# Performance work log

Hardware: AMD Instinct MI355X
Metric: run time of the kernel (lower is better)

## Reference

```python
import jax, jax.numpy as jnp
import numpy as np

N = 25000      # nodes
E = 400000     # edges (before self loops)
G = 64         # graphs in batch
H = 16         # attention heads
ITER = 10      # stacked main GATv2 layers


def setup_inputs():
    key = jax.random.key(0)
    c = [0]
    def nk():
        c[0] += 1
        return jax.random.fold_in(key, c[0])
    def glorot(shape):
        fan = shape[-2] + shape[-1]
        return jax.random.normal(nk(), shape, jnp.float32) * np.float32(np.sqrt(2.0 / fan))
    inp = {
        "x": jax.random.normal(nk(), (N, 2), jnp.float32),
        "edge_attr": jax.random.normal(nk(), (E, 2), jnp.float32),
        "edge_index": jax.random.randint(nk(), (2, E), 0, N, jnp.int32),
        "mask": jax.random.randint(nk(), (N,), 0, 2, jnp.int32),
        "batch": jnp.sort(jax.random.randint(nk(), (N,), 0, G, jnp.int32)),
        # gcn: GATv2Conv(2, 4, heads=16, edge_dim=2), concat -> 64
        "g0_Wl": glorot((2, 64)), "g0_bl": jnp.zeros((64,), jnp.float32),
        "g0_Wr": glorot((2, 64)), "g0_br": jnp.zeros((64,), jnp.float32),
        "g0_We": glorot((2, 64)), "g0_att": glorot((H, 4)),
        "g0_bias": jnp.zeros((64,), jnp.float32),
        "bn_gamma": jnp.ones((64,), jnp.float32),
        "bn_beta": jnp.zeros((64,), jnp.float32),
        "m_Wl": glorot((ITER, 64, 64)), "m_bl": jnp.zeros((ITER, 64), jnp.float32),
        "m_Wr": glorot((ITER, 64, 64)), "m_br": jnp.zeros((ITER, 64), jnp.float32),
        "m_We": glorot((ITER, 2, 64)), "m_att": glorot((ITER, H, 4)),
        "m_bias": jnp.zeros((ITER, 64), jnp.float32),
        # final: GATv2Conv(64, 1, heads=16, concat=False)
        "f_Wl": glorot((64, 16)), "f_bl": jnp.zeros((16,), jnp.float32),
        "f_Wr": glorot((64, 16)), "f_br": jnp.zeros((16,), jnp.float32),
        "f_We": glorot((2, 16)), "f_att": glorot((H, 1)),
        "f_bias": jnp.zeros((1,), jnp.float32),
        # sbs: GATv2Conv(64, 1, heads=16, concat=False)
        "s_Wl": glorot((64, 16)), "s_bl": jnp.zeros((16,), jnp.float32),
        "s_Wr": glorot((64, 16)), "s_br": jnp.zeros((16,), jnp.float32),
        "s_We": glorot((2, 16)), "s_att": glorot((H, 1)),
        "s_bias": jnp.zeros((1,), jnp.float32),
    }
    return inp


def _gatv2(x, src, dst, eattr, Wl, bl, Wr, br, We, att, bias, concat):
    """PyG GATv2Conv: x_l[j]+x_r[i]+e -> LeakyReLU(0.2) -> att dot -> segment softmax over dst."""
    n = x.shape[0]
    h, c = att.shape
    xl = (x @ Wl + bl).reshape(n, h, c)
    xr = (x @ Wr + br).reshape(n, h, c)
    e = (eattr @ We).reshape(-1, h, c)
    m = jax.nn.leaky_relu(xl[src] + xr[dst] + e, 0.2)          # [Etot,H,C]
    logit = jnp.einsum('ehc,hc->eh', m, att)                    # [Etot,H]
    lmax = jax.ops.segment_max(logit, dst, num_segments=n)
    ex = jnp.exp(logit - lmax[dst])
    den = jax.ops.segment_sum(ex, dst, num_segments=n)
    alpha = ex / den[dst]
    out = jax.ops.segment_sum(xl[src] * alpha[..., None], dst, num_segments=n)  # [N,H,C]
    out = out.reshape(n, h * c) if concat else out.mean(axis=1)
    return out + bias


def reference(x, edge_attr, edge_index, mask, batch,
              g0_Wl, g0_bl, g0_Wr, g0_br, g0_We, g0_att, g0_bias,
              bn_gamma, bn_beta,
              m_Wl, m_bl, m_Wr, m_br, m_We, m_att, m_bias,
              f_Wl, f_bl, f_Wr, f_br, f_We, f_att, f_bias,
              s_Wl, s_bl, s_Wr, s_br, s_We, s_att, s_bias):
    n = x.shape[0]
    src, dst = edge_index[0], edge_index[1]
    # add self loops; self-loop edge attr = mean of incoming edge attrs (fill_value='mean')
    ones = jnp.ones((src.shape[0],), jnp.float32)
    cnt = jax.ops.segment_sum(ones, dst, num_segments=n)
    esum = jax.ops.segment_sum(edge_attr, dst, num_segments=n)
    loop_attr = esum / jnp.maximum(cnt, 1.0)[:, None]
    arng = jnp.arange(n, dtype=edge_index.dtype)
    src2 = jnp.concatenate([src, arng])
    dst2 = jnp.concatenate([dst, arng])
    ea2 = jnp.concatenate([edge_attr, loop_attr], axis=0)

    h0 = _gatv2(x, src2, dst2, ea2, g0_Wl, g0_bl, g0_Wr, g0_br, g0_We, g0_att, g0_bias, True)
    mu = h0.mean(axis=0)
    var = h0.var(axis=0)
    h = jax.nn.leaky_relu((h0 - mu) * jax.lax.rsqrt(var + 1e-5) * bn_gamma + bn_beta, 0.01)

    def step(hc, p):
        Wl, bl, Wr, br, We, att, bias = p
        hc = jax.nn.leaky_relu(_gatv2(hc, src2, dst2, ea2, Wl, bl, Wr, br, We, att, bias, True), 0.01)
        return hc, None
    h, _ = jax.lax.scan(step, h, (m_Wl, m_bl, m_Wr, m_br, m_We, m_att, m_bias))

    mus = _gatv2(h, src2, dst2, ea2, s_Wl, s_bl, s_Wr, s_br, s_We, s_att, s_bias, False)[:, 0]  # [N]
    fin = _gatv2(h, src2, dst2, ea2, f_Wl, f_bl, f_Wr, f_br, f_We, f_att, f_bias, False)        # [N,1]
    w = (mask == 0).astype(jnp.float32)
    sums = jax.ops.segment_sum(fin * w[:, None], batch, num_segments=G)
    cnts = jax.ops.segment_sum(w, batch, num_segments=G)
    sat = (sums / jnp.maximum(cnts, 1.0)[:, None])[:, 0]  # [G]
    return mus, sat
```

## Files before the change

### kernel.cpp

```cpp
#include <hip/hip_runtime.h>


static __device__ __forceinline__ float lrelu(float x, float s) {
    return x > 0.f ? x : s * x;
}

__global__ void k_build0(const int* __restrict__ dst, int* __restrict__ cnt,
                         int* __restrict__ rank, int E,
                         const float* __restrict__ x,
                         const float* __restrict__ Wl, const float* __restrict__ bl,
                         const float* __restrict__ Wr, const float* __restrict__ br,
                         float* __restrict__ xl, float* __restrict__ xr, int n) {
    int idx = blockIdx.x * blockDim.x + threadIdx.x;
    if (idx < E) {
        rank[idx] = atomicAdd(&cnt[dst[idx]], 1);
    } else {
        int t = idx - E;
        if (t < n * 64) {
            int i = t >> 6, c = t & 63;
            float x0 = x[2 * i], x1 = x[2 * i + 1];
            xl[t] = x0 * Wl[c] + x1 * Wl[64 + c] + bl[c];
            xr[t] = x0 * Wr[c] + x1 * Wr[64 + c] + br[c];
        }
    }
}

__global__ void k_segoff(const int* __restrict__ cnt, int* __restrict__ row_start,
                         int* __restrict__ cursor, int n) {
    int i = blockIdx.x * blockDim.x + threadIdx.x;
    int lane = threadIdx.x & 63;
    int v = (i < n) ? cnt[i] : 0;
    int s = v;
#pragma unroll
    for (int off = 1; off < 64; off <<= 1) {
        int t = __shfl_up(s, off);
        if (lane >= off) s += t;
    }
    int wavetot = __shfl(s, 63);
    int base = 0;
    if (lane == 63) base = atomicAdd(cursor, wavetot);
    base = __shfl(base, 63);
    if (i < n) row_start[i] = base + s - v;
}

__global__ void k_scatter(const int* __restrict__ src, const int* __restrict__ dst,
                          const float* __restrict__ ea, const int* __restrict__ rank,
                          const int* __restrict__ row_start,
                          int* __restrict__ csr_src, float* __restrict__ csr_ea, int E) {
    int e = blockIdx.x * blockDim.x + threadIdx.x;
    if (e >= E) return;
    int pos = row_start[dst[e]] + rank[e];
    csr_src[pos] = src[e];
    *(float2*)(csr_ea + 2 * (size_t)pos) = *(const float2*)(ea + 2 * (size_t)e);
}

__launch_bounds__(256)
__global__ void k_proj64(const float* __restrict__ h,
                         const float* __restrict__ Wl, const float* __restrict__ bl,
                         const float* __restrict__ Wr, const float* __restrict__ br,
                         const double* __restrict__ stats,
                         const float* __restrict__ bng, const float* __restrict__ bnb,
                         float* __restrict__ xl, float* __restrict__ xr, int n) {
    __shared__ float wsl[4096], wsr[4096], bna[64], bnbb[64];
    int t = threadIdx.x;
    for (int i = t; i < 4096; i += 256) { wsl[i] = Wl[i]; wsr[i] = Wr[i]; }
    if (t < 64) {
        double mu = stats[t] / n;
        double var = stats[64 + t] / n - mu * mu;
        float rs = (float)(1.0 / sqrt(var + 1e-5));
        float a = rs * bng[t];
        bna[t] = a;
        bnbb[t] = bnb[t] - (float)mu * a;
    }
    __syncthreads();
    int rg = t >> 2, cg4 = (t & 3) << 4;
    int r0 = blockIdx.x * 128 + rg * 2;
    float accl[2][16], accr[2][16];
#pragma unroll
    for (int r = 0; r < 2; ++r)
#pragma unroll
        for (int j = 0; j < 16; ++j) { accl[r][j] = 0.f; accr[r][j] = 0.f; }
    for (int k0 = 0; k0 < 64; k0 += 4) {
        float hk[2][4];
#pragma unroll
        for (int r = 0; r < 2; ++r) {
            int gr = r0 + r;
            float4 v = (gr < n) ? *(const float4*)(h + (size_t)gr * 64 + k0)
                                : make_float4(0.f, 0.f, 0.f, 0.f);
            hk[r][0] = v.x; hk[r][1] = v.y; hk[r][2] = v.z; hk[r][3] = v.w;
#pragma unroll
            for (int kk = 0; kk < 4; ++kk)
                hk[r][kk] = lrelu(hk[r][kk] * bna[k0 + kk] + bnbb[k0 + kk], 0.01f);
        }
#pragma unroll
        for (int kk = 0; kk < 4; ++kk) {
            const float* wl = wsl + (k0 + kk) * 64 + cg4;
            const float* wr = wsr + (k0 + kk) * 64 + cg4;
#pragma unroll
            for (int r = 0; r < 2; ++r)
#pragma unroll
                for (int j = 0; j < 16; ++j) {
                    accl[r][j] += hk[r][kk] * wl[j];
                    accr[r][j] += hk[r][kk] * wr[j];
                }
        }
    }
#pragma unroll
    for (int r = 0; r < 2; ++r) {
        int gr = r0 + r;
        if (gr < n) {
            float* ol = xl + (size_t)gr * 64 + cg4;
            float* orr = xr + (size_t)gr * 64 + cg4;
#pragma unroll
            for (int j = 0; j < 16; ++j) {
                ol[j] = accl[r][j] + bl[cg4 + j];
                orr[j] = accr[r][j] + br[cg4 + j];
            }
        }
    }
}

__device__ __forceinline__ float gat_node(const float* __restrict__ xl,
                                          const float* __restrict__ xr,
                                          const int* __restrict__ row_start,
                                          const int* __restrict__ cnt,
                                          const int* __restrict__ csr_src,
                                          const float* __restrict__ csr_ea,
                                          const float* __restrict__ We,
                                          const float* __restrict__ att,
                                          const float* __restrict__ bias,
                                          int d, int lane, int relu) {
    const int p0 = __builtin_amdgcn_readfirstlane(row_start[d]);
    const int deg = __builtin_amdgcn_readfirstlane(cnt[d]);
    const int p1 = p0 + deg;
    const float we0 = We[lane], we1 = We[64 + lane];
    const float av = att[lane];
    const float xrv = xr[(size_t)d * 64 + lane];

    float den0 = 0.f, acc0 = 0.f;
    float den1 = 0.f, acc1 = 0.f;
    float s0 = 0.f, s1 = 0.f;

    auto step = [&](float xv, float2 ea, bool valid, float& den, float& acc) {
        float vm = valid ? 1.f : 0.f;
        s0 = fmaf(vm, ea.x, s0);
        s1 = fmaf(vm, ea.y, s1);
        float tv = lrelu(xv + xrv + ea.x * we0 + ea.y * we1, 0.2f) * av;
        tv += __shfl_xor(tv, 1);
        tv += __shfl_xor(tv, 2);
        if (!valid) tv = -__builtin_inff();
        float w = __expf(tv);
        den += w;
        acc += w * xv;
    };

    for (int p = p0; p < p1; p += 4) {
        int q1 = min(p + 1, p1 - 1), q2 = min(p + 2, p1 - 1), q3 = min(p + 3, p1 - 1);
        int e0s = csr_src[p], e1s = csr_src[q1], e2s = csr_src[q2], e3s = csr_src[q3];
        float2 e0 = *(const float2*)(csr_ea + 2 * (size_t)p);
        float2 e1 = *(const float2*)(csr_ea + 2 * (size_t)q1);
        float2 e2 = *(const float2*)(csr_ea + 2 * (size_t)q2);
        float2 e3 = *(const float2*)(csr_ea + 2 * (size_t)q3);
        float x0 = xl[(size_t)e0s * 64 + lane];
        float x1 = xl[(size_t)e1s * 64 + lane];
        float x2 = xl[(size_t)e2s * 64 + lane];
        float x3 = xl[(size_t)e3s * 64 + lane];
        step(x0, e0, true, den0, acc0);
        step(x1, e1, p + 1 < p1, den1, acc1);
        step(x2, e2, p + 2 < p1, den0, acc0);
        step(x3, e3, p + 3 < p1, den1, acc1);
    }
    {
        float c = fmaxf((float)deg, 1.f);
        float se0 = s0 / c, se1 = s1 / c;
        float xv = xl[(size_t)d * 64 + lane];
        float tv = lrelu(xv + xrv + se0 * we0 + se1 * we1, 0.2f) * av;
        tv += __shfl_xor(tv, 1);
        tv += __shfl_xor(tv, 2);
        float w = __expf(tv);
        den0 += w;
        acc0 += w * xv;
    }
    float o = (acc0 + acc1) / (den0 + den1) + bias[lane];
    if (relu) o = lrelu(o, 0.01f);
    return o;
}

__launch_bounds__(256)
__global__ void k_gat(const float* __restrict__ xl, const float* __restrict__ xr,
                      const int* __restrict__ row_start, const int* __restrict__ cnt,
                      const int* __restrict__ csr_src, const float* __restrict__ csr_ea,
                      const float* __restrict__ We, const float* __restrict__ att,
                      const float* __restrict__ bias,
                      float* __restrict__ out, int n, int relu) {
    int wave = (blockIdx.x * blockDim.x + threadIdx.x) >> 6;
    int lane = threadIdx.x & 63;
    if (wave >= n) return;
    float o = gat_node(xl, xr, row_start, cnt, csr_src, csr_ea, We, att, bias, wave, lane, relu);
    out[(size_t)wave * 64 + lane] = o;
}

__launch_bounds__(256, 8)
__global__ void k_gat_proj2(const float* __restrict__ xl, const float* __restrict__ xr,
                            const int* __restrict__ row_start, const int* __restrict__ cnt,
                            const int* __restrict__ csr_src, const float* __restrict__ csr_ea,
                            const float* __restrict__ We, const float* __restrict__ att,
                            const float* __restrict__ bias,
                            const float* __restrict__ Wnl, const float* __restrict__ bnl,
                            const float* __restrict__ Wnr, const float* __restrict__ bnr,
                            float* __restrict__ xl_out, float* __restrict__ xr_out, int n) {
    int wave = (blockIdx.x * blockDim.x + threadIdx.x) >> 6;
    int lane = threadIdx.x & 63;
    int d0 = wave * 2, d1 = d0 + 1;
    if (d0 >= n) return;
    float o0 = gat_node(xl, xr, row_start, cnt, csr_src, csr_ea, We, att, bias, d0, lane, 1);
    float o1 = (d1 < n)
                   ? gat_node(xl, xr, row_start, cnt, csr_src, csr_ea, We, att, bias, d1, lane, 1)
                   : 0.f;
    float al0a = 0.f, al0b = 0.f, ar0a = 0.f, ar0b = 0.f;
    float al1a = 0.f, al1b = 0.f, ar1a = 0.f, ar1b = 0.f;
#pragma unroll 4
    for (int k = 0; k < 64; k += 2) {
        float h0a = __shfl(o0, k), h0b = __shfl(o0, k + 1);
        float h1a = __shfl(o1, k), h1b = __shfl(o1, k + 1);
        float wl0 = Wnl[k * 64 + lane], wl1 = Wnl[(k + 1) * 64 + lane];
        float wr0 = Wnr[k * 64 + lane], wr1 = Wnr[(k + 1) * 64 + lane];
        al0a += h0a * wl0; al0b += h0b * wl1;
        ar0a += h0a * wr0; ar0b += h0b * wr1;
        al1a += h1a * wl0; al1b += h1b * wl1;
        ar1a += h1a * wr0; ar1b += h1b * wr1;
    }
    float bL = bnl[lane], bR = bnr[lane];
    xl_out[(size_t)d0 * 64 + lane] = al0a + al0b + bL;
    xr_out[(size_t)d0 * 64 + lane] = ar0a + ar0b + bR;
    if (d1 < n) {
        xl_out[(size_t)d1 * 64 + lane] = al1a + al1b + bL;
        xr_out[(size_t)d1 * 64 + lane] = ar1a + ar1b + bR;
    }
}

__launch_bounds__(256, 8)
__global__ void k_gat_projfin2(const float* __restrict__ xl, const float* __restrict__ xr,
                               const int* __restrict__ row_start, const int* __restrict__ cnt,
                               const int* __restrict__ csr_src, const float* __restrict__ csr_ea,
                               const float* __restrict__ We, const float* __restrict__ att,
                               const float* __restrict__ bias,
                               const float* __restrict__ fWl, const float* __restrict__ fbl,
                               const float* __restrict__ fWr, const float* __restrict__ fbr,
                               const float* __restrict__ sWl, const float* __restrict__ sbl,
                               const float* __restrict__ sWr, const float* __restrict__ sbr,
                               float* __restrict__ packed, int n) {
    int wave = (blockIdx.x * blockDim.x + threadIdx.x) >> 6;
    int lane = threadIdx.x & 63;
    int d0 = wave * 2, d1 = d0 + 1;
    if (d0 >= n) return;
    float o0 = gat_node(xl, xr, row_start, cnt, csr_src, csr_ea, We, att, bias, d0, lane, 1);
    float o1 = (d1 < n)
                   ? gat_node(xl, xr, row_start, cnt, csr_src, csr_ea, We, att, bias, d1, lane, 1)
                   : 0.f;
    int q = lane >> 4, cc = lane & 15;
    const float* W = (q == 0) ? fWl : (q == 1) ? sWl : (q == 2) ? fWr : sWr;
    const float* B = (q == 0) ? fbl : (q == 1) ? sbl : (q == 2) ? fbr : sbr;
    float a0 = 0.f, a1 = 0.f, b0 = 0.f, b1 = 0.f;
#pragma unroll 4
    for (int k = 0; k < 64; k += 2) {
        float w0 = W[k * 16 + cc], w1 = W[(k + 1) * 16 + cc];
        a0 += __shfl(o0, k) * w0;
        a1 += __shfl(o0, k + 1) * w1;
        b0 += __shfl(o1, k) * w0;
        b1 += __shfl(o1, k + 1) * w1;
    }
    float bb = B[cc];
    packed[(size_t)d0 * 64 + lane] = a0 + a1 + bb;
    if (d1 < n) packed[(size_t)d1 * 64 + lane] = b0 + b1 + bb;
}

__launch_bounds__(256)
__global__ void k_gat_final(const float* __restrict__ packed,
                            const int* __restrict__ row_start, const int* __restrict__ cnt,
                            const int* __restrict__ csr_src, const float* __restrict__ csr_ea,
                            const float* __restrict__ fWe, const float* __restrict__ sWe,
                            const float* __restrict__ fatt, const float* __restrict__ satt,
                            const float* __restrict__ fbias, const float* __restrict__ sbias,
                            float* __restrict__ fin, float* __restrict__ mus, int n) {
    int hw = (blockIdx.x * blockDim.x + threadIdx.x) >> 5;
    if (hw >= n) return;
    int l = threadIdx.x & 31;
    int hh = l & 15, sel = l >> 4;
    const int d = hw;
    const int p0 = row_start[d], deg = cnt[d], p1 = p0 + deg;
    const float* We = sel ? sWe : fWe;
    float we0 = We[hh], we1 = We[16 + hh];
    float av = (sel ? satt : fatt)[hh];
    float xrv = packed[(size_t)d * 64 + 32 + sel * 16 + hh];
    int xli = sel * 16 + hh;

    float den0 = 0.f, acc0 = 0.f;
    float den1 = 0.f, acc1 = 0.f;
    float s0 = 0.f, s1 = 0.f;

    auto step = [&](float xv, float2 ea, bool valid, float& den, float& acc) {
        float vm = valid ? 1.f : 0.f;
        s0 = fmaf(vm, ea.x, s0);
        s1 = fmaf(vm, ea.y, s1);
        float t = lrelu(xv + xrv + ea.x * we0 + ea.y * we1, 0.2f) * av;
        if (!valid) t = -__builtin_inff();
        float w = __expf(t);
        den += w;
        acc += w * xv;
    };

    for (int p = p0; p < p1; p += 4) {
        int q1 = min(p + 1, p1 - 1), q2 = min(p + 2, p1 - 1), q3 = min(p + 3, p1 - 1);
        int e0s = csr_src[p], e1s = csr_src[q1], e2s = csr_src[q2], e3s = csr_src[q3];
        float2 e0 = *(const float2*)(csr_ea + 2 * (size_t)p);
        float2 e1 = *(const float2*)(csr_ea + 2 * (size_t)q1);
        float2 e2 = *(const float2*)(csr_ea + 2 * (size_t)q2);
        float2 e3 = *(const float2*)(csr_ea + 2 * (size_t)q3);
        float x0 = packed[(size_t)e0s * 64 + xli];
        float x1 = packed[(size_t)e1s * 64 + xli];
        float x2 = packed[(size_t)e2s * 64 + xli];
        float x3 = packed[(size_t)e3s * 64 + xli];
        step(x0, e0, true, den0, acc0);
        step(x1, e1, p + 1 < p1, den1, acc1);
        step(x2, e2, p + 2 < p1, den0, acc0);
        step(x3, e3, p + 3 < p1, den1, acc1);
    }
    {
        float c = fmaxf((float)deg, 1.f);
        float se0 = s0 / c, se1 = s1 / c;
        float xv = packed[(size_t)d * 64 + xli];
        float t = lrelu(xv + xrv + se0 * we0 + se1 * we1, 0.2f) * av;
        float w = __expf(t);
        den0 += w;
        acc0 += w * xv;
    }
    float val = (acc0 + acc1) / (den0 + den1);
#pragma unroll
    for (int w = 1; w < 16; w <<= 1) val += __shfl_xor(val, w);
    if ((threadIdx.x & 15) == 0) {
        float o = val * (1.f / 16.f) + (sel ? sbias[0] : fbias[0]);
        if (sel) mus[d] = o; else fin[d] = o;
    }
}


__global__ void k_bnstats(const float* __restrict__ h, double* __restrict__ stats, int n) {
    int c = threadIdx.x & 63;
    int s0 = blockIdx.x * (blockDim.x >> 6) + (threadIdx.x >> 6);
    int ns = gridDim.x * (blockDim.x >> 6);
    double s = 0.0, s2 = 0.0;
    for (int i = s0; i < n; i += ns) {
        float v = h[(size_t)i * 64 + c];
        s += v;
        s2 += (double)v * v;
    }
    atomicAdd(&stats[c], s);
    atomicAdd(&stats[64 + c], s2);
}


__global__ void k_sat_acc(const float* __restrict__ fin, const int* __restrict__ mask,
                          const int* __restrict__ batch,
                          float* __restrict__ sums, float* __restrict__ cnts, int n) {
    int i = blockIdx.x * blockDim.x + threadIdx.x;
    int lane = threadIdx.x & 63;
    int g = (i < n) ? batch[i] : -1;
    float c = (i < n && mask[i] == 0) ? 1.f : 0.f;
    float v = (c > 0.f) ? fin[i] : 0.f;
#pragma unroll
    for (int off = 1; off < 64; off <<= 1) {
        float v2 = __shfl_down(v, off);
        float c2 = __shfl_down(c, off);
        int g2 = __shfl_down(g, off);
        if (lane + off < 64 && g2 == g) { v += v2; c += c2; }
    }
    int gprev = __shfl_up(g, 1);
    bool head = (lane == 0) || (gprev != g);
    if (head && g >= 0 && c > 0.f) {
        atomicAdd(&sums[g], v);
        atomicAdd(&cnts[g], c);
    }
}

__global__ void k_sat_fin(const float* __restrict__ sums, const float* __restrict__ cnts,
                          float* __restrict__ out, int g) {
    int i = threadIdx.x;
    if (i < g) out[i] = sums[i] / fmaxf(cnts[i], 1.f);
}


extern "C" void kernel_launch(void* const* d_in, const int* in_sizes, int n_in,
                              void* d_out, int out_size, void* d_ws, size_t ws_size,
                              hipStream_t stream) {
    const float* x = (const float*)d_in[0];
    const float* eat = (const float*)d_in[1];
    const int* ei = (const int*)d_in[2];
    const int* mask = (const int*)d_in[3];
    const int* batch = (const int*)d_in[4];
    const float* g0_Wl = (const float*)d_in[5];
    const float* g0_bl = (const float*)d_in[6];
    const float* g0_Wr = (const float*)d_in[7];
    const float* g0_br = (const float*)d_in[8];
    const float* g0_We = (const float*)d_in[9];
    const float* g0_att = (const float*)d_in[10];
    const float* g0_bias = (const float*)d_in[11];
    const float* bn_g = (const float*)d_in[12];
    const float* bn_b = (const float*)d_in[13];
    const float* m_Wl = (const float*)d_in[14];
    const float* m_bl = (const float*)d_in[15];
    const float* m_Wr = (const float*)d_in[16];
    const float* m_br = (const float*)d_in[17];
    const float* m_We = (const float*)d_in[18];
    const float* m_att = (const float*)d_in[19];
    const float* m_bias = (const float*)d_in[20];
    const float* f_Wl = (const float*)d_in[21];
    const float* f_bl = (const float*)d_in[22];
    const float* f_Wr = (const float*)d_in[23];
    const float* f_br = (const float*)d_in[24];
    const float* f_We = (const float*)d_in[25];
    const float* f_att = (const float*)d_in[26];
    const float* f_bias = (const float*)d_in[27];
    const float* s_Wl = (const float*)d_in[28];
    const float* s_bl = (const float*)d_in[29];
    const float* s_Wr = (const float*)d_in[30];
    const float* s_br = (const float*)d_in[31];
    const float* s_We = (const float*)d_in[32];
    const float* s_att = (const float*)d_in[33];
    const float* s_bias = (const float*)d_in[34];

    const int N = in_sizes[3];
    const int E = in_sizes[1] / 2;
    const int G = out_size - N;
    const int ITER = in_sizes[14] / 4096;
    const int* srcp = ei;
    const int* dstp = ei + E;

    char* wsb = (char*)d_ws;
    size_t off = 0;
    auto alloc = [&](size_t b) { void* p = wsb + off; off = (off + b + 255) & ~(size_t)255; return p; };
    int* cnt = (int*)alloc((size_t)N * 4);
    int* cursor = (int*)alloc(256);
    double* stats = (double*)alloc(128 * 8);
    float* sums = (float*)alloc((size_t)G * 4);
    float* cnts = (float*)alloc((size_t)G * 4);
    size_t zero_bytes = off;
    int* rank = (int*)alloc((size_t)E * 4);
    int* row_start = (int*)alloc((size_t)N * 4);
    int* csr_src = (int*)alloc((size_t)E * 4);
    float* csr_ea = (float*)alloc((size_t)E * 8);
    float* xlA = (float*)alloc((size_t)N * 256);
    float* xrA = (float*)alloc((size_t)N * 256);
    float* xlB = (float*)alloc((size_t)N * 256);
    float* xrB = (float*)alloc((size_t)N * 256);
    float* hbuf = (float*)alloc((size_t)N * 256);
    float* fin = (float*)alloc((size_t)N * 4);
    (void)ws_size; (void)n_in;

    float* outv = (float*)d_out;

    hipMemsetAsync(d_ws, 0, zero_bytes, stream);
    const int tb = 256;
    const int ggrid = (N * 64 + 255) / 256;
    const int npair = (N + 1) / 2;
    const int ggrid2 = (npair * 64 + 255) / 256;
    k_build0<<<(E + N * 64 + tb - 1) / tb, tb, 0, stream>>>(dstp, cnt, rank, E,
                                                            x, g0_Wl, g0_bl, g0_Wr, g0_br,
                                                            xlA, xrA, N);
    k_segoff<<<(N + tb - 1) / tb, tb, 0, stream>>>(cnt, row_start, cursor, N);
    k_scatter<<<(E + tb - 1) / tb, tb, 0, stream>>>(srcp, dstp, eat, rank, row_start,
                                                    csr_src, csr_ea, E);

    k_gat<<<ggrid, tb, 0, stream>>>(xlA, xrA, row_start, cnt, csr_src, csr_ea,
                                    g0_We, g0_att, g0_bias, hbuf, N, 0);
    k_bnstats<<<128, 256, 0, stream>>>(hbuf, stats, N);
    k_proj64<<<(N + 127) / 128, 256, 0, stream>>>(hbuf, m_Wl, m_bl, m_Wr, m_br,
                                                  stats, bn_g, bn_b, xlA, xrA, N);

    float* cur_l = xlA; float* cur_r = xrA;
    float* alt_l = xlB; float* alt_r = xrB;
    for (int l = 0; l < ITER; ++l) {
        if (l < ITER - 1) {
            k_gat_proj2<<<ggrid2, tb, 0, stream>>>(cur_l, cur_r, row_start, cnt, csr_src, csr_ea,
                                                   m_We + l * 128, m_att + l * 64, m_bias + l * 64,
                                                   m_Wl + (size_t)(l + 1) * 4096, m_bl + (l + 1) * 64,
                                                   m_Wr + (size_t)(l + 1) * 4096, m_br + (l + 1) * 64,
                                                   alt_l, alt_r, N);
        } else {
            k_gat_projfin2<<<ggrid2, tb, 0, stream>>>(cur_l, cur_r, row_start, cnt, csr_src, csr_ea,
                                                      m_We + l * 128, m_att + l * 64, m_bias + l * 64,
                                                      f_Wl, f_bl, f_Wr, f_br,
                                                      s_Wl, s_bl, s_Wr, s_br,
                                                      alt_l, N);
        }
        float* t;
        t = cur_l; cur_l = alt_l; alt_l = t;
        t = cur_r; cur_r = alt_r; alt_r = t;
    }
    k_gat_final<<<(N * 32 + tb - 1) / tb, tb, 0, stream>>>(cur_l, row_start, cnt, csr_src, csr_ea,
                                                           f_We, s_We, f_att, s_att,
                                                           f_bias, s_bias, fin, outv, N);
    k_sat_acc<<<(N + tb - 1) / tb, tb, 0, stream>>>(fin, mask, batch, sums, cnts, N);
    k_sat_fin<<<1, 64, 0, stream>>>(sums, cnts, outv + N, G);
}
```

Before: 630.2 us.

## Interleave edge loops of two destination nodes per wave for more memory parallelism

Replaces the per-node aggregation with a two-node routine that walks the edge lists of both destinations in lockstep, issuing eight independent gathers per iteration instead of four. The aim is more memory-level parallelism to hide gather latency in the GAT layers. The first layer also switches to two nodes per wave, and the leaky ReLU becomes a branchless max. In exchange the loop runs to the larger of the two degrees with masked work, uses more registers, and pads the CSR arrays with a sentinel entry.

```diff
diff --git a/kernel.cpp b/kernel.cpp
--- a/kernel.cpp
+++ b/kernel.cpp
@@ -2,7 +2,7 @@
 
 
 static __device__ __forceinline__ float lrelu(float x, float s) {
-    return x > 0.f ? x : s * x;
+    return fmaxf(x, s * x);
 }
 
 __global__ void k_build0(const int* __restrict__ dst, int* __restrict__ cnt,
@@ -48,6 +48,11 @@
                           const int* __restrict__ row_start,
                           int* __restrict__ csr_src, float* __restrict__ csr_ea, int E) {
     int e = blockIdx.x * blockDim.x + threadIdx.x;
+    if (blockIdx.x == 0 && threadIdx.x == 0) {
+        csr_src[E] = 0;
+        csr_ea[2 * (size_t)E] = 0.f;
+        csr_ea[2 * (size_t)E + 1] = 0.f;
+    }
     if (e >= E) return;
     int pos = row_start[dst[e]] + rank[e];
     csr_src[pos] = src[e];
@@ -120,7 +125,7 @@
     }
 }
 
-__device__ __forceinline__ float gat_node(const float* __restrict__ xl,
+__device__ __forceinline__ void gat_node2(const float* __restrict__ xl,
                                           const float* __restrict__ xr,
                                           const int* __restrict__ row_start,
                                           const int* __restrict__ cnt,
@@ -129,19 +134,23 @@
                                           const float* __restrict__ We,
                                           const float* __restrict__ att,
                                           const float* __restrict__ bias,
-                                          int d, int lane, int relu) {
-    const int p0 = __builtin_amdgcn_readfirstlane(row_start[d]);
-    const int deg = __builtin_amdgcn_readfirstlane(cnt[d]);
-    const int p1 = p0 + deg;
+                                          int d0, int d1, int lane, int relu,
+                                          float& out0, float& out1) {
+    const int p0a = __builtin_amdgcn_readfirstlane(row_start[d0]);
+    const int dega = __builtin_amdgcn_readfirstlane(cnt[d0]);
+    const int p0b = __builtin_amdgcn_readfirstlane(row_start[d1]);
+    const int degb = __builtin_amdgcn_readfirstlane(cnt[d1]);
+    const int p1a = p0a + dega, p1b = p0b + degb;
     const float we0 = We[lane], we1 = We[64 + lane];
     const float av = att[lane];
-    const float xrv = xr[(size_t)d * 64 + lane];
-
-    float den0 = 0.f, acc0 = 0.f;
-    float den1 = 0.f, acc1 = 0.f;
-    float s0 = 0.f, s1 = 0.f;
-
-    auto step = [&](float xv, float2 ea, bool valid, float& den, float& acc) {
+    const float xrva = xr[((size_t)d0 << 6) + lane];
+    const float xrvb = xr[((size_t)d1 << 6) + lane];
+
+    float denA0 = 0.f, accA0 = 0.f, denA1 = 0.f, accA1 = 0.f, sA0 = 0.f, sA1 = 0.f;
+    float denB0 = 0.f, accB0 = 0.f, denB1 = 0.f, accB1 = 0.f, sB0 = 0.f, sB1 = 0.f;
+
+    auto step = [&](float xv, float xrv, float2 ea, bool valid,
+                    float& den, float& acc, float& s0, float& s1) {
         float vm = valid ? 1.f : 0.f;
         s0 = fmaf(vm, ea.x, s0);
         s1 = fmaf(vm, ea.y, s1);
@@ -154,50 +163,80 @@
         acc += w * xv;
     };
 
-    for (int p = p0; p < p1; p += 4) {
-        int q1 = min(p + 1, p1 - 1), q2 = min(p + 2, p1 - 1), q3 = min(p + 3, p1 - 1);
-        int e0s = csr_src[p], e1s = csr_src[q1], e2s = csr_src[q2], e3s = csr_src[q3];
-        float2 e0 = *(const float2*)(csr_ea + 2 * (size_t)p);
-        float2 e1 = *(const float2*)(csr_ea + 2 * (size_t)q1);
-        float2 e2 = *(const float2*)(csr_ea + 2 * (size_t)q2);
-        float2 e3 = *(const float2*)(csr_ea + 2 * (size_t)q3);
-        float x0 = xl[(size_t)e0s * 64 + lane];
-        float x1 = xl[(size_t)e1s * 64 + lane];
-        float x2 = xl[(size_t)e2s * 64 + lane];
-        float x3 = xl[(size_t)e3s * 64 + lane];
-        step(x0, e0, true, den0, acc0);
-        step(x1, e1, p + 1 < p1, den1, acc1);
-        step(x2, e2, p + 2 < p1, den0, acc0);
-        step(x3, e3, p + 3 < p1, den1, acc1);
+    const int iters = max(dega, degb);
+    for (int base = 0; base < iters; base += 4) {
+        const int pa = p0a + base, pb = p0b + base;
+        int ia[4], ib[4];
+        float2 ea4[4], eb4[4];
+#pragma unroll
+        for (int j = 0; j < 4; ++j) {
+            int qa = max(min(pa + j, p1a - 1), p0a);
+            int qb = max(min(pb + j, p1b - 1), p0b);
+            ia[j] = csr_src[qa];
+            ib[j] = csr_src[qb];
+            ea4[j] = *(const float2*)(csr_ea + 2 * (size_t)qa);
+            eb4[j] = *(const float2*)(csr_ea + 2 * (size_t)qb);
+        }
+        float xa[4], xb[4];
+#pragma unroll
+        for (int j = 0; j < 4; ++j) {
+            xa[j] = xl[(unsigned)((ia[j] << 6) + lane)];
+            xb[j] = xl[(unsigned)((ib[j] << 6) + lane)];
+        }
+        step(xa[0], xrva, ea4[0], base + 0 < dega, denA0, accA0, sA0, sA1);
+        step(xb[0], xrvb, eb4[0], base + 0 < degb, denB0, accB0, sB0, sB1);
+        step(xa[1], xrva, ea4[1], base + 1 < dega, denA1, accA1, sA0, sA1);
+        step(xb[1], xrvb, eb4[1], base + 1 < degb, denB1, accB1, sB0, sB1);
+        step(xa[2], xrva, ea4[2], base + 2 < dega, denA0, accA0, sA0, sA1);
+        step(xb[2], xrvb, eb4[2], base + 2 < degb, denB0, accB0, sB0, sB1);
+        step(xa[3], xrva, ea4[3], base + 3 < dega, denA1, accA1, sA0, sA1);
+        step(xb[3], xrvb, eb4[3], base + 3 < degb, denB1, accB1, sB0, sB1);
     }
     {
-        float c = fmaxf((float)deg, 1.f);
-        float se0 = s0 / c, se1 = s1 / c;
-        float xv = xl[(size_t)d * 64 + lane];
-        float tv = lrelu(xv + xrv + se0 * we0 + se1 * we1, 0.2f) * av;
+        float c = fmaxf((float)dega, 1.f);
+        float se0 = sA0 / c, se1 = sA1 / c;
+        float xv = xl[((size_t)d0 << 6) + lane];
+        float tv = lrelu(xv + xrva + se0 * we0 + se1 * we1, 0.2f) * av;
         tv += __shfl_xor(tv, 1);
         tv += __shfl_xor(tv, 2);
         float w = __expf(tv);
-        den0 += w;
-        acc0 += w * xv;
-    }
-    float o = (acc0 + acc1) / (den0 + den1) + bias[lane];
-    if (relu) o = lrelu(o, 0.01f);
-    return o;
-}
-
-__launch_bounds__(256)
-__global__ void k_gat(const float* __restrict__ xl, const float* __restrict__ xr,
-                      const int* __restrict__ row_start, const int* __restrict__ cnt,
-                      const int* __restrict__ csr_src, const float* __restrict__ csr_ea,
-                      const float* __restrict__ We, const float* __restrict__ att,
-                      const float* __restrict__ bias,
-                      float* __restrict__ out, int n, int relu) {
+        denA0 += w;
+        accA0 += w * xv;
+    }
+    {
+        float c = fmaxf((float)degb, 1.f);
+        float se0 = sB0 / c, se1 = sB1 / c;
+        float xv = xl[((size_t)d1 << 6) + lane];
+        float tv = lrelu(xv + xrvb + se0 * we0 + se1 * we1, 0.2f) * av;
+        tv += __shfl_xor(tv, 1);
+        tv += __shfl_xor(tv, 2);
+        float w = __expf(tv);
+        denB0 += w;
+        accB0 += w * xv;
+    }
+    float o0 = (accA0 + accA1) / (denA0 + denA1) + bias[lane];
+    float o1 = (accB0 + accB1) / (denB0 + denB1) + bias[lane];
+    if (relu) { o0 = lrelu(o0, 0.01f); o1 = lrelu(o1, 0.01f); }
+    out0 = o0;
+    out1 = o1;
+}
+
+__launch_bounds__(256, 8)
+__global__ void k_gat2(const float* __restrict__ xl, const float* __restrict__ xr,
+                       const int* __restrict__ row_start, const int* __restrict__ cnt,
+                       const int* __restrict__ csr_src, const float* __restrict__ csr_ea,
+                       const float* __restrict__ We, const float* __restrict__ att,
+                       const float* __restrict__ bias,
+                       float* __restrict__ out, int n, int relu) {
     int wave = (blockIdx.x * blockDim.x + threadIdx.x) >> 6;
     int lane = threadIdx.x & 63;
-    if (wave >= n) return;
-    float o = gat_node(xl, xr, row_start, cnt, csr_src, csr_ea, We, att, bias, wave, lane, relu);
-    out[(size_t)wave * 64 + lane] = o;
+    int d0 = wave * 2;
+    if (d0 >= n) return;
+    int d1 = min(d0 + 1, n - 1);
+    float o0, o1;
+    gat_node2(xl, xr, row_start, cnt, csr_src, csr_ea, We, att, bias, d0, d1, lane, relu, o0, o1);
+    out[((size_t)d0 << 6) + lane] = o0;
+    if (d0 + 1 < n) out[((size_t)d1 << 6) + lane] = o1;
 }
 
 __launch_bounds__(256, 8)
@@ -211,12 +250,11 @@
                             float* __restrict__ xl_out, float* __restrict__ xr_out, int n) {
     int wave = (blockIdx.x * blockDim.x + threadIdx.x) >> 6;
     int lane = threadIdx.x & 63;
-    int d0 = wave * 2, d1 = d0 + 1;
+    int d0 = wave * 2;
     if (d0 >= n) return;
-    float o0 = gat_node(xl, xr, row_start, cnt, csr_src, csr_ea, We, att, bias, d0, lane, 1);
-    float o1 = (d1 < n)
-                   ? gat_node(xl, xr, row_start, cnt, csr_src, csr_ea, We, att, bias, d1, lane, 1)
-                   : 0.f;
+    int d1 = min(d0 + 1, n - 1);
+    float o0, o1;
+    gat_node2(xl, xr, row_start, cnt, csr_src, csr_ea, We, att, bias, d0, d1, lane, 1, o0, o1);
     float al0a = 0.f, al0b = 0.f, ar0a = 0.f, ar0b = 0.f;
     float al1a = 0.f, al1b = 0.f, ar1a = 0.f, ar1b = 0.f;
 #pragma unroll 4
@@ -231,11 +269,11 @@
         ar1a += h1a * wr0; ar1b += h1b * wr1;
     }
     float bL = bnl[lane], bR = bnr[lane];
-    xl_out[(size_t)d0 * 64 + lane] = al0a + al0b + bL;
-    xr_out[(size_t)d0 * 64 + lane] = ar0a + ar0b + bR;
-    if (d1 < n) {
-        xl_out[(size_t)d1 * 64 + lane] = al1a + al1b + bL;
-        xr_out[(size_t)d1 * 64 + lane] = ar1a + ar1b + bR;
+    xl_out[((size_t)d0 << 6) + lane] = al0a + al0b + bL;
+    xr_out[((size_t)d0 << 6) + lane] = ar0a + ar0b + bR;
+    if (d0 + 1 < n) {
+        xl_out[((size_t)d1 << 6) + lane] = al1a + al1b + bL;
+        xr_out[((size_t)d1 << 6) + lane] = ar1a + ar1b + bR;
     }
 }
 
@@ -252,12 +290,11 @@
                                float* __restrict__ packed, int n) {
     int wave = (blockIdx.x * blockDim.x + threadIdx.x) >> 6;
     int lane = threadIdx.x & 63;
-    int d0 = wave * 2, d1 = d0 + 1;
+    int d0 = wave * 2;
     if (d0 >= n) return;
-    float o0 = gat_node(xl, xr, row_start, cnt, csr_src, csr_ea, We, att, bias, d0, lane, 1);
-    float o1 = (d1 < n)
-                   ? gat_node(xl, xr, row_start, cnt, csr_src, csr_ea, We, att, bias, d1, lane, 1)
-                   : 0.f;
+    int d1 = min(d0 + 1, n - 1);
+    float o0, o1;
+    gat_node2(xl, xr, row_start, cnt, csr_src, csr_ea, We, att, bias, d0, d1, lane, 1, o0, o1);
     int q = lane >> 4, cc = lane & 15;
     const float* W = (q == 0) ? fWl : (q == 1) ? sWl : (q == 2) ? fWr : sWr;
     const float* B = (q == 0) ? fbl : (q == 1) ? sbl : (q == 2) ? fbr : sbr;
@@ -271,8 +308,8 @@
         b1 += __shfl(o1, k + 1) * w1;
     }
     float bb = B[cc];
-    packed[(size_t)d0 * 64 + lane] = a0 + a1 + bb;
-    if (d1 < n) packed[(size_t)d1 * 64 + lane] = b0 + b1 + bb;
+    packed[((size_t)d0 << 6) + lane] = a0 + a1 + bb;
+    if (d0 + 1 < n) packed[((size_t)d1 << 6) + lane] = b0 + b1 + bb;
 }
 
 __launch_bounds__(256)
@@ -447,8 +484,8 @@
     size_t zero_bytes = off;
     int* rank = (int*)alloc((size_t)E * 4);
     int* row_start = (int*)alloc((size_t)N * 4);
-    int* csr_src = (int*)alloc((size_t)E * 4);
-    float* csr_ea = (float*)alloc((size_t)E * 8);
+    int* csr_src = (int*)alloc((size_t)(E + 4) * 4);
+    float* csr_ea = (float*)alloc((size_t)(E + 4) * 8);
     float* xlA = (float*)alloc((size_t)N * 256);
     float* xrA = (float*)alloc((size_t)N * 256);
     float* xlB = (float*)alloc((size_t)N * 256);
@@ -461,7 +498,6 @@
 
     hipMemsetAsync(d_ws, 0, zero_bytes, stream);
     const int tb = 256;
-    const int ggrid = (N * 64 + 255) / 256;
     const int npair = (N + 1) / 2;
     const int ggrid2 = (npair * 64 + 255) / 256;
     k_build0<<<(E + N * 64 + tb - 1) / tb, tb, 0, stream>>>(dstp, cnt, rank, E,
@@ -471,8 +507,8 @@
     k_scatter<<<(E + tb - 1) / tb, tb, 0, stream>>>(srcp, dstp, eat, rank, row_start,
                                                     csr_src, csr_ea, E);
 
-    k_gat<<<ggrid, tb, 0, stream>>>(xlA, xrA, row_start, cnt, csr_src, csr_ea,
-                                    g0_We, g0_att, g0_bias, hbuf, N, 0);
+    k_gat2<<<ggrid2, tb, 0, stream>>>(xlA, xrA, row_start, cnt, csr_src, csr_ea,
+                                      g0_We, g0_att, g0_bias, hbuf, N, 0);
     k_bnstats<<<128, 256, 0, stream>>>(hbuf, stats, N);
     k_proj64<<<(N + 127) / 128, 256, 0, stream>>>(hbuf, m_Wl, m_bl, m_Wr, m_br,
                                                   stats, bn_g, bn_b, xlA, xrA, N);
```

Result: slower. 663.2 us (+5.2%).

## Fuse first-layer projection into GAT0 and launch main layers with 64-thread blocks

Applied to the files above, without the earlier changes.

The first GATv2 layer now computes the 2-to-64 projections on the fly from the raw 2-dim node features inside a new k_gat0 kernel. This removes the separate xl/xr materialization in k_build0 and the 64-float gathers per edge, replacing them with 8-byte feature gathers plus a few FMAs. The main-layer kernels change from 256-thread blocks to one 64-thread block per node pair, which may change scheduling granularity. Smaller edits swap lrelu to fmaxf, use shift-based indexing, and pad the CSR buffers.

```diff
diff --git a/kernel.cpp b/kernel.cpp
--- a/kernel.cpp
+++ b/kernel.cpp
@@ -2,27 +2,13 @@
 
 
 static __device__ __forceinline__ float lrelu(float x, float s) {
-    return x > 0.f ? x : s * x;
+    return fmaxf(x, s * x);
 }
 
 __global__ void k_build0(const int* __restrict__ dst, int* __restrict__ cnt,
-                         int* __restrict__ rank, int E,
-                         const float* __restrict__ x,
-                         const float* __restrict__ Wl, const float* __restrict__ bl,
-                         const float* __restrict__ Wr, const float* __restrict__ br,
-                         float* __restrict__ xl, float* __restrict__ xr, int n) {
+                         int* __restrict__ rank, int E) {
     int idx = blockIdx.x * blockDim.x + threadIdx.x;
-    if (idx < E) {
-        rank[idx] = atomicAdd(&cnt[dst[idx]], 1);
-    } else {
-        int t = idx - E;
-        if (t < n * 64) {
-            int i = t >> 6, c = t & 63;
-            float x0 = x[2 * i], x1 = x[2 * i + 1];
-            xl[t] = x0 * Wl[c] + x1 * Wl[64 + c] + bl[c];
-            xr[t] = x0 * Wr[c] + x1 * Wr[64 + c] + br[c];
-        }
-    }
+    if (idx < E) rank[idx] = atomicAdd(&cnt[dst[idx]], 1);
 }
 
 __global__ void k_segoff(const int* __restrict__ cnt, int* __restrict__ row_start,
@@ -52,6 +38,78 @@
     int pos = row_start[dst[e]] + rank[e];
     csr_src[pos] = src[e];
     *(float2*)(csr_ea + 2 * (size_t)pos) = *(const float2*)(ea + 2 * (size_t)e);
+}
+
+__launch_bounds__(256, 8)
+__global__ void k_gat0(const float* __restrict__ x,
+                       const int* __restrict__ row_start, const int* __restrict__ cnt,
+                       const int* __restrict__ csr_src, const float* __restrict__ csr_ea,
+                       const float* __restrict__ Wl, const float* __restrict__ bl,
+                       const float* __restrict__ Wr, const float* __restrict__ br,
+                       const float* __restrict__ We, const float* __restrict__ att,
+                       const float* __restrict__ bias,
+                       float* __restrict__ out, int n) {
+    int d = (blockIdx.x * blockDim.x + threadIdx.x) >> 6;
+    int lane = threadIdx.x & 63;
+    if (d >= n) return;
+    const int p0 = __builtin_amdgcn_readfirstlane(row_start[d]);
+    const int deg = __builtin_amdgcn_readfirstlane(cnt[d]);
+    const int p1 = p0 + deg;
+    const float wl0 = Wl[lane], wl1 = Wl[64 + lane], blv = bl[lane];
+    const float we0 = We[lane], we1 = We[64 + lane];
+    const float av = att[lane];
+    const float2 xd = *(const float2*)(x + 2 * (size_t)d);
+    const float xrv = fmaf(xd.x, Wr[lane], fmaf(xd.y, Wr[64 + lane], br[lane]));
+
+    float den0 = 0.f, acc0 = 0.f;
+    float den1 = 0.f, acc1 = 0.f;
+    float s0 = 0.f, s1 = 0.f;
+
+    auto step = [&](float xv, float2 ea, bool valid, float& den, float& acc) {
+        float vm = valid ? 1.f : 0.f;
+        s0 = fmaf(vm, ea.x, s0);
+        s1 = fmaf(vm, ea.y, s1);
+        float tv = lrelu(xv + xrv + ea.x * we0 + ea.y * we1, 0.2f) * av;
+        tv += __shfl_xor(tv, 1);
+        tv += __shfl_xor(tv, 2);
+        if (!valid) tv = -__builtin_inff();
+        float w = __expf(tv);
+        den += w;
+        acc += w * xv;
+    };
+
+    for (int p = p0; p < p1; p += 4) {
+        int q1 = min(p + 1, p1 - 1), q2 = min(p + 2, p1 - 1), q3 = min(p + 3, p1 - 1);
+        int e0s = csr_src[p], e1s = csr_src[q1], e2s = csr_src[q2], e3s = csr_src[q3];
+        float2 ea0 = *(const float2*)(csr_ea + 2 * (size_t)p);
+        float2 ea1 = *(const float2*)(csr_ea + 2 * (size_t)q1);
+        float2 ea2 = *(const float2*)(csr_ea + 2 * (size_t)q2);
+        float2 ea3 = *(const float2*)(csr_ea + 2 * (size_t)q3);
+        float2 xs0 = *(const float2*)(x + 2 * (size_t)e0s);
+        float2 xs1 = *(const float2*)(x + 2 * (size_t)e1s);
+        float2 xs2 = *(const float2*)(x + 2 * (size_t)e2s);
+        float2 xs3 = *(const float2*)(x + 2 * (size_t)e3s);
+        float xv0 = fmaf(xs0.x, wl0, fmaf(xs0.y, wl1, blv));
+        float xv1 = fmaf(xs1.x, wl0, fmaf(xs1.y, wl1, blv));
+        float xv2 = fmaf(xs2.x, wl0, fmaf(xs2.y, wl1, blv));
+        float xv3 = fmaf(xs3.x, wl0, fmaf(xs3.y, wl1, blv));
+        step(xv0, ea0, true, den0, acc0);
+        step(xv1, ea1, p + 1 < p1, den1, acc1);
+        step(xv2, ea2, p + 2 < p1, den0, acc0);
+        step(xv3, ea3, p + 3 < p1, den1, acc1);
+    }
+    {
+        float c = fmaxf((float)deg, 1.f);
+        float se0 = s0 / c, se1 = s1 / c;
+        float xv = fmaf(xd.x, wl0, fmaf(xd.y, wl1, blv));
+        float tv = lrelu(xv + xrv + se0 * we0 + se1 * we1, 0.2f) * av;
+        tv += __shfl_xor(tv, 1);
+        tv += __shfl_xor(tv, 2);
+        float w = __expf(tv);
+        den0 += w;
+        acc0 += w * xv;
+    }
+    out[((size_t)d << 6) + lane] = (acc0 + acc1) / (den0 + den1) + bias[lane];
 }
 
 __launch_bounds__(256)
@@ -135,7 +193,7 @@
     const int p1 = p0 + deg;
     const float we0 = We[lane], we1 = We[64 + lane];
     const float av = att[lane];
-    const float xrv = xr[(size_t)d * 64 + lane];
+    const float xrv = xr[((size_t)d << 6) + lane];
 
     float den0 = 0.f, acc0 = 0.f;
     float den1 = 0.f, acc1 = 0.f;
@@ -161,10 +219,10 @@
         float2 e1 = *(const float2*)(csr_ea + 2 * (size_t)q1);
         float2 e2 = *(const float2*)(csr_ea + 2 * (size_t)q2);
         float2 e3 = *(const float2*)(csr_ea + 2 * (size_t)q3);
-        float x0 = xl[(size_t)e0s * 64 + lane];
-        float x1 = xl[(size_t)e1s * 64 + lane];
-        float x2 = xl[(size_t)e2s * 64 + lane];
-        float x3 = xl[(size_t)e3s * 64 + lane];
+        float x0 = xl[((size_t)e0s << 6) + lane];
+        float x1 = xl[((size_t)e1s << 6) + lane];
+        float x2 = xl[((size_t)e2s << 6) + lane];
+        float x3 = xl[((size_t)e3s << 6) + lane];
         step(x0, e0, true, den0, acc0);
         step(x1, e1, p + 1 < p1, den1, acc1);
         step(x2, e2, p + 2 < p1, den0, acc0);
@@ -173,7 +231,7 @@
     {
         float c = fmaxf((float)deg, 1.f);
         float se0 = s0 / c, se1 = s1 / c;
-        float xv = xl[(size_t)d * 64 + lane];
+        float xv = xl[((size_t)d << 6) + lane];
         float tv = lrelu(xv + xrv + se0 * we0 + se1 * we1, 0.2f) * av;
         tv += __shfl_xor(tv, 1);
         tv += __shfl_xor(tv, 2);
@@ -186,21 +244,7 @@
     return o;
 }
 
-__launch_bounds__(256)
-__global__ void k_gat(const float* __restrict__ xl, const float* __restrict__ xr,
-                      const int* __restrict__ row_start, const int* __restrict__ cnt,
-                      const int* __restrict__ csr_src, const float* __restrict__ csr_ea,
-                      const float* __restrict__ We, const float* __restrict__ att,
-                      const float* __restrict__ bias,
-                      float* __restrict__ out, int n, int relu) {
-    int wave = (blockIdx.x * blockDim.x + threadIdx.x) >> 6;
-    int lane = threadIdx.x & 63;
-    if (wave >= n) return;
-    float o = gat_node(xl, xr, row_start, cnt, csr_src, csr_ea, We, att, bias, wave, lane, relu);
-    out[(size_t)wave * 64 + lane] = o;
-}
-
-__launch_bounds__(256, 8)
+__launch_bounds__(64, 8)
 __global__ void k_gat_proj2(const float* __restrict__ xl, const float* __restrict__ xr,
                             const int* __restrict__ row_start, const int* __restrict__ cnt,
                             const int* __restrict__ csr_src, const float* __restrict__ csr_ea,
@@ -209,7 +253,7 @@
                             const float* __restrict__ Wnl, const float* __restrict__ bnl,
                             const float* __restrict__ Wnr, const float* __restrict__ bnr,
                             float* __restrict__ xl_out, float* __restrict__ xr_out, int n) {
-    int wave = (blockIdx.x * blockDim.x + threadIdx.x) >> 6;
+    int wave = blockIdx.x;
     int lane = threadIdx.x & 63;
     int d0 = wave * 2, d1 = d0 + 1;
     if (d0 >= n) return;
@@ -231,15 +275,15 @@
         ar1a += h1a * wr0; ar1b += h1b * wr1;
     }
     float bL = bnl[lane], bR = bnr[lane];
-    xl_out[(size_t)d0 * 64 + lane] = al0a + al0b + bL;
-    xr_out[(size_t)d0 * 64 + lane] = ar0a + ar0b + bR;
+    xl_out[((size_t)d0 << 6) + lane] = al0a + al0b + bL;
+    xr_out[((size_t)d0 << 6) + lane] = ar0a + ar0b + bR;
     if (d1 < n) {
-        xl_out[(size_t)d1 * 64 + lane] = al1a + al1b + bL;
-        xr_out[(size_t)d1 * 64 + lane] = ar1a + ar1b + bR;
-    }
-}
-
-__launch_bounds__(256, 8)
+        xl_out[((size_t)d1 << 6) + lane] = al1a + al1b + bL;
+        xr_out[((size_t)d1 << 6) + lane] = ar1a + ar1b + bR;
+    }
+}
+
+__launch_bounds__(64, 8)
 __global__ void k_gat_projfin2(const float* __restrict__ xl, const float* __restrict__ xr,
                                const int* __restrict__ row_start, const int* __restrict__ cnt,
                                const int* __restrict__ csr_src, const float* __restrict__ csr_ea,
@@ -250,7 +294,7 @@
                                const float* __restrict__ sWl, const float* __restrict__ sbl,
                                const float* __restrict__ sWr, const float* __restrict__ sbr,
                                float* __restrict__ packed, int n) {
-    int wave = (blockIdx.x * blockDim.x + threadIdx.x) >> 6;
+    int wave = blockIdx.x;
     int lane = threadIdx.x & 63;
     int d0 = wave * 2, d1 = d0 + 1;
     if (d0 >= n) return;
@@ -271,8 +315,8 @@
         b1 += __shfl(o1, k + 1) * w1;
     }
     float bb = B[cc];
-    packed[(size_t)d0 * 64 + lane] = a0 + a1 + bb;
-    if (d1 < n) packed[(size_t)d1 * 64 + lane] = b0 + b1 + bb;
+    packed[((size_t)d0 << 6) + lane] = a0 + a1 + bb;
+    if (d1 < n) packed[((size_t)d1 << 6) + lane] = b0 + b1 + bb;
 }
 
 __launch_bounds__(256)
@@ -447,8 +491,8 @@
     size_t zero_bytes = off;
     int* rank = (int*)alloc((size_t)E * 4);
     int* row_start = (int*)alloc((size_t)N * 4);
-    int* csr_src = (int*)alloc((size_t)E * 4);
-    float* csr_ea = (float*)alloc((size_t)E * 8);
+    int* csr_src = (int*)alloc((size_t)(E + 4) * 4);
+    float* csr_ea = (float*)alloc((size_t)(E + 4) * 8);
     float* xlA = (float*)alloc((size_t)N * 256);
     float* xrA = (float*)alloc((size_t)N * 256);
     float* xlB = (float*)alloc((size_t)N * 256);
@@ -463,16 +507,14 @@
     const int tb = 256;
     const int ggrid = (N * 64 + 255) / 256;
     const int npair = (N + 1) / 2;
-    const int ggrid2 = (npair * 64 + 255) / 256;
-    k_build0<<<(E + N * 64 + tb - 1) / tb, tb, 0, stream>>>(dstp, cnt, rank, E,
-                                                            x, g0_Wl, g0_bl, g0_Wr, g0_br,
-                                                            xlA, xrA, N);
+    k_build0<<<(E + tb - 1) / tb, tb, 0, stream>>>(dstp, cnt, rank, E);
     k_segoff<<<(N + tb - 1) / tb, tb, 0, stream>>>(cnt, row_start, cursor, N);
     k_scatter<<<(E + tb - 1) / tb, tb, 0, stream>>>(srcp, dstp, eat, rank, row_start,
                                                     csr_src, csr_ea, E);
 
-    k_gat<<<ggrid, tb, 0, stream>>>(xlA, xrA, row_start, cnt, csr_src, csr_ea,
-                                    g0_We, g0_att, g0_bias, hbuf, N, 0);
+    k_gat0<<<ggrid, tb, 0, stream>>>(x, row_start, cnt, csr_src, csr_ea,
+                                     g0_Wl, g0_bl, g0_Wr, g0_br,
+                                     g0_We, g0_att, g0_bias, hbuf, N);
     k_bnstats<<<128, 256, 0, stream>>>(hbuf, stats, N);
     k_proj64<<<(N + 127) / 128, 256, 0, stream>>>(hbuf, m_Wl, m_bl, m_Wr, m_br,
                                                   stats, bn_g, bn_b, xlA, xrA, N);
@@ -481,17 +523,17 @@
     float* alt_l = xlB; float* alt_r = xrB;
     for (int l = 0; l < ITER; ++l) {
         if (l < ITER - 1) {
-            k_gat_proj2<<<ggrid2, tb, 0, stream>>>(cur_l, cur_r, row_start, cnt, csr_src, csr_ea,
-                                                   m_We + l * 128, m_att + l * 64, m_bias + l * 64,
-                                                   m_Wl + (size_t)(l + 1) * 4096, m_bl + (l + 1) * 64,
-                                                   m_Wr + (size_t)(l + 1) * 4096, m_br + (l + 1) * 64,
-                                                   alt_l, alt_r, N);
+            k_gat_proj2<<<npair, 64, 0, stream>>>(cur_l, cur_r, row_start, cnt, csr_src, csr_ea,
+                                                  m_We + l * 128, m_att + l * 64, m_bias + l * 64,
+                                                  m_Wl + (size_t)(l + 1) * 4096, m_bl + (l + 1) * 64,
+                                                  m_Wr + (size_t)(l + 1) * 4096, m_br + (l + 1) * 64,
+                                                  alt_l, alt_r, N);
         } else {
-            k_gat_projfin2<<<ggrid2, tb, 0, stream>>>(cur_l, cur_r, row_start, cnt, csr_src, csr_ea,
-                                                      m_We + l * 128, m_att + l * 64, m_bias + l * 64,
-                                                      f_Wl, f_bl, f_Wr, f_br,
-                                                      s_Wl, s_bl, s_Wr, s_br,
-                                                      alt_l, N);
+            k_gat_projfin2<<<npair, 64, 0, stream>>>(cur_l, cur_r, row_start, cnt, csr_src, csr_ea,
+                                                     m_We + l * 128, m_att + l * 64, m_bias + l * 64,
+                                                     f_Wl, f_bl, f_Wr, f_br,
+                                                     s_Wl, s_bl, s_Wr, s_br,
+                                                     alt_l, N);
         }
         float* t;
         t = cur_l; cur_l = alt_l; alt_l = t;
```

After: 627.3 us. Within noise of the previous version (-0.5%).
